# Kernel optimization log

Measured on AMD Instinct MI355X. Metric: run time of the kernel, lower is better.

Reference implementation:

```python
import jax, jax.numpy as jnp
import numpy as np

B, N, KS = 4, 4096, 16  # ks = int(k * random_rate) = int(20 * 0.8)
EPS = 1e-5


def bn_relu(x):
    # training-mode BatchNorm (stats over all dims but channel=last) + ReLU
    ax = tuple(range(x.ndim - 1))
    m = x.mean(ax, keepdims=True)
    v = x.var(ax, keepdims=True)
    return jax.nn.relu((x - m) * jax.lax.rsqrt(v + EPS))


def knn_idx(points, ks):
    # points: [B,N,3] -> neighbor indices [B,N,ks] (self included)
    sq = jnp.sum(points * points, -1)
    d2 = sq[:, :, None] + sq[:, None, :] - 2.0 * jnp.einsum('bnd,bmd->bnm', points, points)
    _, idx = jax.lax.top_k(-d2, ks)
    return idx


def gather(f, idx):
    # f: [B,N,C], idx: [B,N,k] -> [B,N,k,C]
    return jax.vmap(lambda ff, ii: ff[ii])(f, idx)


def edge_conv(feat, idx, W, pts=None):
    # EdgeConv: concat(x_i, x_j - x_i [, p_j - p_i]) -> 1x1 conv -> BN+ReLU -> max_k
    nb = gather(feat, idx)                       # [B,N,k,C]
    c = feat[:, :, None, :]
    e = jnp.concatenate([jnp.broadcast_to(c, nb.shape), nb - c], -1)
    if pts is not None:
        e = jnp.concatenate([e, gather(pts, idx) - pts[:, :, None, :]], -1)
    h = jnp.einsum('bnkc,cd->bnkd', e, W)
    return bn_relu(h).max(2)                     # [B,N,out]


def graph_conv(feat, idx, W):
    agg = gather(feat, idx).max(2)               # [B,N,C]
    return bn_relu(agg @ W)


def forward(data, W_fc, b_fc, W1, W2, W3, W4, W5, W6, W10, W11, W12, W13):
    pts = data[..., :3]
    idx = knn_idx(pts, KS)                       # [B,N,KS]
    x0 = bn_relu(data @ W_fc + b_fc)             # fc_start + bn_start, [B,N,64]
    x = edge_conv(x0, idx, W1, pts=pts)          # spFEM 64 -> 256 (edge dim 131)
    x = graph_conv(x, idx, W2)                   # 256 -> 64
    x = graph_conv(x, idx, W3)                   # 64 -> 64
    x1 = x
    x = edge_conv(x, idx, W4)                    # FEM 64 -> 256 (edge dim 128)
    x = graph_conv(x, idx, W5)                   # 256 -> 64
    x = graph_conv(x, idx, W6)                   # 64 -> 64
    x2 = x
    # (conv7..conv90 produce x3/x4 which the head never consumes -> skipped)
    x12 = jnp.concatenate([x1, x2], -1)          # [B,N,128]
    h = bn_relu(x12 @ W10)                       # conv10: 128 -> 1024
    g = h.max(1)                                 # global max pool, [B,1024]
    cat = jnp.concatenate([jnp.broadcast_to(g[:, None, :], (B, N, 1024)), x1, x2], -1)  # [B,N,1152]
    h = bn_relu(cat @ W11)                       # conv11: 1152 -> 512
    h = bn_relu(h @ W12)                         # conv12: 512 -> 256
    out = h @ W13                                # conv13: 256 -> 13 (dropout = identity in eval)
    return out.transpose(0, 2, 1)                # [B,13,N]


def setup_inputs() -> dict:
    key = jax.random.key(0)
    ks = jax.random.split(key, 16)
    w = lambda k, *s: jax.random.normal(k, s, jnp.float32) * 0.05
    return {
        'data': jax.random.normal(ks[0], (B, N, 9), jnp.float32),
        'W_fc': w(ks[1], 9, 64), 'b_fc': jnp.zeros((64,), jnp.float32),
        'W1': w(ks[2], 131, 256),   # 2*64 + 3 (sp variant adds p_j - p_i)
        'W2': w(ks[3], 256, 64), 'W3': w(ks[4], 64, 64),
        'W4': w(ks[5], 128, 256),   # 2*64
        'W5': w(ks[6], 256, 64), 'W6': w(ks[7], 64, 64),
        'W10': w(ks[8], 128, 1024), 'W11': w(ks[9], 1152, 512),
        'W12': w(ks[10], 512, 256), 'W13': w(ks[11], 256, 13),
    }


def reference(data, W_fc, b_fc, W1, W2, W3, W4, W5, W6, W10, W11, W12, W13):
    return forward(data, W_fc, b_fc, W1, W2, W3, W4, W5, W6, W10, W11, W12, W13)
```

## Files before the change

### kernel.cpp

```cpp
#include <hip/hip_runtime.h>
#include <hip/hip_bf16.h>
#include <float.h>

static constexpr int BB  = 4;
static constexpr int NN  = 4096;
static constexpr int KSN = 16;
static constexpr int RN  = BB * NN;
#define EPSBN 1e-5f

typedef __attribute__((ext_vector_type(8))) short short8;
typedef __attribute__((ext_vector_type(4))) short short4v;
typedef __attribute__((ext_vector_type(4))) float f32x4;

__device__ inline unsigned short f2bf(float f) {
  union { float f; unsigned u; } v; v.f = f;
  unsigned r = v.u + 0x7FFF + ((v.u >> 16) & 1);
  return (unsigned short)(r >> 16);
}
__device__ inline float bf2f(unsigned short h) {
  union { unsigned u; float f; } v; v.u = ((unsigned)h) << 16; return v.f;
}

__global__ __launch_bounds__(256) void prepgram_kernel(const float* __restrict__ data,
                                                       float4* __restrict__ pack,
                                                       float* __restrict__ partials) {
  const int t = blockIdx.x * 256 + threadIdx.x;
  const int lane = threadIdx.x & 63, wave = threadIdx.x >> 6;
  __shared__ float red[4][54];
  float d[9];
#pragma unroll
  for (int k = 0; k < 9; ++k) d[k] = data[(size_t)t * 9 + k];
  pack[t] = make_float4(d[0], d[1], d[2], fmaf(d[2], d[2], fmaf(d[1], d[1], d[0] * d[0])));
  int p = 0;
#pragma unroll
  for (int i = 0; i < 9; ++i) {
    float v = d[i];
#pragma unroll
    for (int mv = 1; mv < 64; mv <<= 1) v += __shfl_xor(v, mv);
    if (lane == 0) red[wave][p] = v;
    ++p;
  }
#pragma unroll
  for (int i = 0; i < 9; ++i)
#pragma unroll
    for (int j = i; j < 9; ++j) {
      float v = d[i] * d[j];
#pragma unroll
      for (int mv = 1; mv < 64; mv <<= 1) v += __shfl_xor(v, mv);
      if (lane == 0) red[wave][p] = v;
      ++p;
    }
  __syncthreads();
  if (threadIdx.x < 54)
    partials[blockIdx.x * 54 + threadIdx.x] =
        red[0][threadIdx.x] + red[1][threadIdx.x] + red[2][threadIdx.x] + red[3][threadIdx.x];
}

__global__ void fcstats_kernel(const float* __restrict__ partials,
                               const float* __restrict__ W, const float* __restrict__ bias,
                               float* __restrict__ S0) {
  __shared__ float g[54];
  const int t = threadIdx.x;
  if (t < 54) {
    float s = 0.f;
    for (int b = 0; b < 64; ++b) s += partials[b * 54 + t];
    g[t] = s;
  }
  __syncthreads();
  float w[9];
#pragma unroll
  for (int k = 0; k < 9; ++k) w[k] = W[k * 64 + t];
  float b = bias[t];
  float dotw = 0.f;
#pragma unroll
  for (int k = 0; k < 9; ++k) dotw = fmaf(g[k], w[k], dotw);
  float s2 = 0.f;
  int p = 9;
#pragma unroll
  for (int i = 0; i < 9; ++i)
#pragma unroll
    for (int j = i; j < 9; ++j) {
      float gij = g[p++];
      s2 = fmaf(gij * ((i == j) ? 1.f : 2.f), w[i] * w[j], s2);
    }
  s2 += 2.f * b * dotw + (float)RN * b * b;
  S0[t] = dotw + (float)RN * b;
  S0[64 + t] = s2;
}

__device__ inline void wpack_one(const float* __restrict__ W, unsigned short* __restrict__ wh,
                                 unsigned short* __restrict__ wl, int t, int lgC, int NK) {
  int k = t >> lgC, c = t & ((1 << lgC) - 1);
  float v = W[t];
  int ct = c >> 4, cl = c & 15, ks = k >> 5, kl = k & 31;
  int dst = ((ct * NK + ks) * 64 + (((kl >> 3) << 4) | cl)) * 8 + (kl & 7);
  unsigned short h = f2bf(v);
  wh[dst] = h; wl[dst] = f2bf(v - bf2f(h));
}
__device__ inline void diffpack_one(const float* __restrict__ W, unsigned short* __restrict__ wh,
                                    unsigned short* __restrict__ wl, int t) {
  int k = t >> 8, cc = t & 255;
  float v = W[k * 256 + cc] - W[(64 + k) * 256 + cc];
  int ct = cc >> 4, cl = cc & 15, ks = k >> 5, kl = k & 31;
  int dst = ((ct * 2 + ks) * 64 + (((kl >> 3) << 4) | cl)) * 8 + (kl & 7);
  unsigned short h = f2bf(v);
  wh[dst] = h; wl[dst] = f2bf(v - bf2f(h));
}

__global__ __launch_bounds__(256) void mega_kernel(
    const float4* __restrict__ pack, int* __restrict__ idx,
    const float* __restrict__ data, const float* __restrict__ W_fc,
    const float* __restrict__ b_fc, const float* __restrict__ S0,
    unsigned short* __restrict__ xbh, unsigned short* __restrict__ xbl,
    const float* __restrict__ W1, const float* __restrict__ W4,
    const float* __restrict__ W2, const float* __restrict__ W3,
    const float* __restrict__ W5, const float* __restrict__ W6,
    const float* __restrict__ W10, const float* __restrict__ W11, const float* __restrict__ W12,
    unsigned short* __restrict__ W1mh, unsigned short* __restrict__ W1ml, float4* __restrict__ W1bt,
    unsigned short* __restrict__ W4mh, unsigned short* __restrict__ W4ml,
    unsigned short* __restrict__ W1ph, unsigned short* __restrict__ W1pl,
    unsigned short* __restrict__ W4ph, unsigned short* __restrict__ W4pl,
    unsigned short* __restrict__ W2h, unsigned short* __restrict__ W2l,
    unsigned short* __restrict__ W3h, unsigned short* __restrict__ W3l,
    unsigned short* __restrict__ W5h, unsigned short* __restrict__ W5l,
    unsigned short* __restrict__ W6h, unsigned short* __restrict__ W6l,
    unsigned short* __restrict__ W10h, unsigned short* __restrict__ W10l,
    unsigned short* __restrict__ W11xh, unsigned short* __restrict__ W11xl,
    unsigned short* __restrict__ W12h, unsigned short* __restrict__ W12l) {
  const int blk = blockIdx.x;
  if (blk < 4096) {
    const int lane = threadIdx.x & 63;
    const int p = blk * 4 + (threadIdx.x >> 6);
    const int b = p >> 12;
    const float4* __restrict__ pb = pack + ((size_t)b << 12);
    const float4 me = pack[p];
    unsigned long long m0 = ~0ull, m1 = ~0ull, m2 = ~0ull, m3 = ~0ull;
#pragma unroll 8
    for (int s = 0; s < 64; ++s) {
      const float4 q = pb[s * 64 + lane];
      float d = me.w + q.w - 2.0f * fmaf(me.x, q.x, fmaf(me.y, q.y, me.z * q.z));
      unsigned ub = __float_as_uint(d);
      ub = (ub & 0x80000000u) ? ~ub : (ub | 0x80000000u);
      unsigned long long k = ((unsigned long long)ub << 12) | (unsigned)(s * 64 + lane);
      if (k < m3) {
        bool l0 = k < m0;  unsigned long long t0 = l0 ? m0 : k;  m0 = l0 ? k : m0;
        bool l1 = t0 < m1; unsigned long long t1 = l1 ? m1 : t0; m1 = l1 ? t0 : m1;
        bool l2 = t1 < m2; unsigned long long t2 = l2 ? m2 : t1; m2 = l2 ? t1 : m2;
        m3 = (t2 < m3) ? t2 : m3;
      }
    }
    for (int pass = 0; pass < 16; ++pass) {
      unsigned d0 = (unsigned)(m0 >> 12);
      unsigned w32 = d0;
#pragma unroll
      for (int mv = 1; mv < 64; mv <<= 1) {
        unsigned o = __shfl_xor(w32, mv);
        w32 = (o < w32) ? o : w32;
      }
      unsigned long long ball = __ballot(d0 == w32);
      unsigned widx;
      if (__popcll(ball) == 1) {
        widx = __shfl((unsigned)(m0 & 0xFFFull), (int)(__ffsll((long long)ball) - 1));
      } else {
        unsigned cand = (d0 == w32) ? (unsigned)(m0 & 0xFFFull) : 0xFFFFFFFFu;
#pragma unroll
        for (int mv = 1; mv < 64; mv <<= 1) {
          unsigned o = __shfl_xor(cand, mv);
          cand = (o < cand) ? o : cand;
        }
        widx = cand;
      }
      const unsigned long long w = ((unsigned long long)w32 << 12) | widx;
      if (lane == pass) idx[(p << 4) + pass] = (int)widx;
      if (m0 == w) { m0 = m1; m1 = m2; m2 = m3; m3 = ~0ull; }
      if (pass < 15 && __any(m0 == ~0ull)) {
        if (m0 == ~0ull) {
          m1 = ~0ull; m2 = ~0ull; m3 = ~0ull;
#pragma unroll 8
          for (int s = 0; s < 64; ++s) {
            const float4 q = pb[s * 64 + lane];
            float d = me.w + q.w - 2.0f * fmaf(me.x, q.x, fmaf(me.y, q.y, me.z * q.z));
            unsigned ub = __float_as_uint(d);
            ub = (ub & 0x80000000u) ? ~ub : (ub | 0x80000000u);
            unsigned long long k = ((unsigned long long)ub << 12) | (unsigned)(s * 64 + lane);
            k = (k > w) ? k : ~0ull;
            if (k < m3) {
              bool l0 = k < m0;  unsigned long long t0 = l0 ? m0 : k;  m0 = l0 ? k : m0;
              bool l1 = t0 < m1; unsigned long long t1 = l1 ? m1 : t0; m1 = l1 ? t0 : m1;
              bool l2 = t1 < m2; unsigned long long t2 = l2 ? m2 : t1; m2 = l2 ? t1 : m2;
              m3 = (t2 < m3) ? t2 : m3;
            }
          }
        }
      }
    }
  } else if (blk < 8192) {
    const int t = (blk - 4096) * 256 + threadIdx.x;
    const int r = t >> 6, c = t & 63;
    const float* dr = data + (size_t)r * 9;
    float acc = b_fc[c];
#pragma unroll
    for (int k = 0; k < 9; ++k) acc = fmaf(dr[k], W_fc[k * 64 + c], acc);
    const float inv = 1.0f / RN;
    float m = S0[c] * inv;
    float v = fmaxf(S0[64 + c] * inv - m * m, 0.0f);
    float x = fmaxf((acc - m) * rsqrtf(v + EPSBN), 0.0f);
    unsigned short h = f2bf(x);
    xbh[t] = h; xbl[t] = f2bf(x - bf2f(h));
  } else {
    const int mb = blk - 8192;
    if (mb < 64) {
      int t = mb * 256 + threadIdx.x;
      int k = t >> 8, cc = t & 255;
      float w1mid = W1[(64 + k) * 256 + cc];
      unsigned short h1 = f2bf(w1mid);
      W1mh[cc * 64 + k] = h1;
      W1ml[cc * 64 + k] = f2bf(w1mid - bf2f(h1));
      float w4mid = W4[(64 + k) * 256 + cc];
      unsigned short h4 = f2bf(w4mid);
      W4mh[cc * 64 + k] = h4;
      W4ml[cc * 64 + k] = f2bf(w4mid - bf2f(h4));
      if (t < 256) W1bt[t] = make_float4(W1[128 * 256 + t], W1[129 * 256 + t], W1[130 * 256 + t], 0.f);
    } else if (mb < 128) {
      diffpack_one(W1, W1ph, W1pl, (mb - 64) * 256 + threadIdx.x);
    } else if (mb < 192) {
      diffpack_one(W4, W4ph, W4pl, (mb - 128) * 256 + threadIdx.x);
    } else if (mb < 256) {
      wpack_one(W2, W2h, W2l, (mb - 192) * 256 + threadIdx.x, 6, 8);
    } else if (mb < 272) {
      wpack_one(W3, W3h, W3l, (mb - 256) * 256 + threadIdx.x, 6, 2);
    } else if (mb < 336) {
      wpack_one(W5, W5h, W5l, (mb - 272) * 256 + threadIdx.x, 6, 8);
    } else if (mb < 352) {
      wpack_one(W6, W6h, W6l, (mb - 336) * 256 + threadIdx.x, 6, 2);
    } else if (mb < 864) {
      wpack_one(W10, W10h, W10l, (mb - 352) * 256 + threadIdx.x, 10, 4);
    } else if (mb < 1120) {
      wpack_one(W11 + 1024 * 512, W11xh, W11xl, (mb - 864) * 256 + threadIdx.x, 9, 4);
    } else {
      wpack_one(W12, W12h, W12l, (mb - 1120) * 256 + threadIdx.x, 8, 16);
    }
  }
}

__global__ void pack_x12_kernel(const float* __restrict__ x1, const float* __restrict__ x2,
                                const float* __restrict__ S6,
                                unsigned short* __restrict__ ph, unsigned short* __restrict__ pl) {
  int t = blockIdx.x * 256 + threadIdx.x;
  int r = t >> 7, k = t & 127;
  float v;
  if (k < 64) {
    v = x1[(size_t)r * 64 + k];
  } else {
    int c = k - 64;
    const float inv = 1.0f / RN;
    float m = S6[c] * inv;
    float var = fmaxf(S6[64 + c] * inv - m * m, 0.f);
    v = fmaxf((x2[(size_t)r * 64 + c] - m) * rsqrtf(var + EPSBN), 0.f);
  }
  int rt = r >> 4, rl = r & 15, ks = k >> 5, kl = k & 31;
  int dst = ((rt * 4 + ks) * 64 + (((kl >> 3) << 4) | rl)) * 8 + (kl & 7);
  unsigned short h = f2bf(v);
  ph[dst] = h; pl[dst] = f2bf(v - bf2f(h));
}

__global__ void bn_pack_kernel(const float* __restrict__ buf, const float* __restrict__ stats,
                               unsigned short* __restrict__ ph, unsigned short* __restrict__ pl) {
  int t = blockIdx.x * 256 + threadIdx.x;
  int c = t & 511, r = t >> 9;
  const float inv = 1.0f / RN;
  float m = stats[c] * inv;
  float v = fmaxf(stats[512 + c] * inv - m * m, 0.0f);
  float x = fmaxf((buf[t] - m) * rsqrtf(v + EPSBN), 0.0f);
  int rt = r >> 4, rl = r & 15, ks = c >> 5, kl = c & 31;
  int dst = ((rt * 16 + ks) * 64 + (((kl >> 3) << 4) | rl)) * 8 + (kl & 7);
  unsigned short h = f2bf(x);
  ph[dst] = h; pl[dst] = f2bf(x - bf2f(h));
}

__global__ void bn_normpack_kernel(float* __restrict__ buf, const float* __restrict__ stats,
                                   unsigned short* __restrict__ hi, unsigned short* __restrict__ lo) {
  int t = blockIdx.x * 256 + threadIdx.x;
  int c = t & 63;
  const float inv = 1.0f / RN;
  float m = stats[c] * inv;
  float v = fmaxf(stats[64 + c] * inv - m * m, 0.0f);
  float x = fmaxf((buf[t] - m) * rsqrtf(v + EPSBN), 0.0f);
  buf[t] = x;
  unsigned short h = f2bf(x);
  hi[t] = h; lo[t] = f2bf(x - bf2f(h));
}

template <bool HAS_PTS>
__global__ __launch_bounds__(256) void edge_mfma_kernel(
    const unsigned short* __restrict__ Xh, const unsigned short* __restrict__ Xl,
    const int* __restrict__ idx,
    const float4* __restrict__ pack,
    const unsigned short* __restrict__ Wmh, const unsigned short* __restrict__ Wml,
    const float4* __restrict__ Wbt, const float* __restrict__ basemat,
    float* __restrict__ out, float* __restrict__ stats) {
  const int wave = threadIdx.x >> 6;
  const int lane = threadIdx.x & 63;
  const int pg   = blockIdx.x;
  const int c0   = wave << 6;
  const int cl   = lane & 15;
  const int kg   = (lane >> 4) << 3;
  const int bat  = pg >> 8;
  const int pbase = bat << 12;
  const int ib   = pg << 8;

  short8 bh[4][2], blo[4][2];
#pragma unroll
  for (int q = 0; q < 4; ++q) {
    const unsigned short* wp = Wmh + (size_t)(c0 + q * 16 + cl) * 64 + kg;
    bh[q][0] = *(const short8*)wp; bh[q][1] = *(const short8*)(wp + 32);
    const unsigned short* wq = Wml + (size_t)(c0 + q * 16 + cl) * 64 + kg;
    blo[q][0] = *(const short8*)wq; blo[q][1] = *(const short8*)(wq + 32);
  }
  float4 wb[4];
  if (HAS_PTS) {
#pragma unroll
    for (int q = 0; q < 4; ++q) wb[q] = Wbt[c0 + q * 16 + cl];
  }
  float P1[4] = {0.f, 0.f, 0.f, 0.f}, P2[4] = {0.f, 0.f, 0.f, 0.f};
  float PCx[4] = {0.f, 0.f, 0.f, 0.f};
  float PB1[4] = {0.f, 0.f, 0.f, 0.f}, PB2[4] = {0.f, 0.f, 0.f, 0.f};

  int jn = idx[ib + 16 + cl];
  int j0 = idx[ib + cl];
  size_t ro = ((size_t)(pbase | j0) << 6) + kg;
  short8 a0h = *(const short8*)(Xh + ro);
  short8 a1h = *(const short8*)(Xh + ro + 32);
  short8 a0l = *(const short8*)(Xl + ro);
  short8 a1l = *(const short8*)(Xl + ro + 32);

  for (int pp = 0; pp < 16; ++pp) {
    const int p = (pg << 4) | pp;
    int jf = 0;
    if (pp < 14) jf = idx[ib + ((pp + 2) << 4) + cl];
    short8 n0h, n1h, n0l, n1l;
    if (pp < 15) {
      size_t rn = ((size_t)(pbase | jn) << 6) + kg;
      n0h = *(const short8*)(Xh + rn);
      n1h = *(const short8*)(Xh + rn + 32);
      n0l = *(const short8*)(Xl + rn);
      n1l = *(const short8*)(Xl + rn + 32);
    }
    float dx0, dy0, dz0, dx1, dy1, dz1, dx2, dy2, dz2, dx3, dy3, dz3;
    if (HAS_PTS) {
      const int4 j4 = *(const int4*)(idx + (p << 4) + ((lane >> 4) << 2));
      const float4 pc = pack[p];
      const float4 q0 = pack[pbase | j4.x];
      const float4 q1 = pack[pbase | j4.y];
      const float4 q2 = pack[pbase | j4.z];
      const float4 q3 = pack[pbase | j4.w];
      dx0 = q0.x - pc.x; dy0 = q0.y - pc.y; dz0 = q0.z - pc.z;
      dx1 = q1.x - pc.x; dy1 = q1.y - pc.y; dz1 = q1.z - pc.z;
      dx2 = q2.x - pc.x; dy2 = q2.y - pc.y; dz2 = q2.z - pc.z;
      dx3 = q3.x - pc.x; dy3 = q3.y - pc.y; dz3 = q3.z - pc.z;
    }
    f32x4 acc[4];
#pragma unroll
    for (int q = 0; q < 4; ++q) {
      acc[q][0] = 0.f; acc[q][1] = 0.f; acc[q][2] = 0.f; acc[q][3] = 0.f;
    }
#pragma unroll
    for (int q = 0; q < 4; ++q) {
      acc[q] = __builtin_amdgcn_mfma_f32_16x16x32_bf16(a0l, bh[q][0], acc[q], 0, 0, 0);
      acc[q] = __builtin_amdgcn_mfma_f32_16x16x32_bf16(a1l, bh[q][1], acc[q], 0, 0, 0);
      acc[q] = __builtin_amdgcn_mfma_f32_16x16x32_bf16(a0h, blo[q][0], acc[q], 0, 0, 0);
      acc[q] = __builtin_amdgcn_mfma_f32_16x16x32_bf16(a1h, blo[q][1], acc[q], 0, 0, 0);
      acc[q] = __builtin_amdgcn_mfma_f32_16x16x32_bf16(a0h, bh[q][0], acc[q], 0, 0, 0);
      acc[q] = __builtin_amdgcn_mfma_f32_16x16x32_bf16(a1h, bh[q][1], acc[q], 0, 0, 0);
    }
    if (HAS_PTS) {
#pragma unroll
      for (int q = 0; q < 4; ++q) {
        acc[q][0] += dx0 * wb[q].x + dy0 * wb[q].y + dz0 * wb[q].z;
        acc[q][1] += dx1 * wb[q].x + dy1 * wb[q].y + dz1 * wb[q].z;
        acc[q][2] += dx2 * wb[q].x + dy2 * wb[q].y + dz2 * wb[q].z;
        acc[q][3] += dx3 * wb[q].x + dy3 * wb[q].y + dz3 * wb[q].z;
      }
    }
#pragma unroll
    for (int q = 0; q < 4; ++q) {
      float s1p = acc[q][0] + acc[q][1] + acc[q][2] + acc[q][3];
      float s2p = acc[q][0] * acc[q][0] + acc[q][1] * acc[q][1]
                + acc[q][2] * acc[q][2] + acc[q][3] * acc[q][3];
      float mx = fmaxf(fmaxf(acc[q][0], acc[q][1]), fmaxf(acc[q][2], acc[q][3]));
      mx = fmaxf(mx, __shfl_xor(mx, 16));
      mx = fmaxf(mx, __shfl_xor(mx, 32));
      float bb = basemat[(size_t)p * 256 + c0 + q * 16 + cl];
      if (lane < 16) out[(size_t)p * 256 + c0 + q * 16 + cl] = mx + bb;
      P1[q] += s1p;
      P2[q] += s2p;
      PCx[q] = fmaf(bb, s1p, PCx[q]);
      PB1[q] += bb;
      PB2[q] = fmaf(bb, bb, PB2[q]);
    }
    a0h = n0h; a1h = n1h; a0l = n0l; a1l = n1l;
    jn = jf;
  }
#pragma unroll
  for (int q = 0; q < 4; ++q) {
    float p1 = P1[q]; p1 += __shfl_xor(p1, 16); p1 += __shfl_xor(p1, 32);
    float p2 = P2[q]; p2 += __shfl_xor(p2, 16); p2 += __shfl_xor(p2, 32);
    float pc = PCx[q]; pc += __shfl_xor(pc, 16); pc += __shfl_xor(pc, 32);
    if (lane < 16) {
      atomicAdd(&stats[c0 + q * 16 + lane], p1 + 16.f * PB1[q]);
      atomicAdd(&stats[256 + c0 + q * 16 + lane], p2 + 2.f * pc + 16.f * PB2[q]);
    }
  }
}

template <int LGC>
__global__ __launch_bounds__(256) void agg_pack_kernel(
    const float* __restrict__ X, const int* __restrict__ idx,
    const float* __restrict__ stats, float inv_cnt,
    unsigned short* __restrict__ ph, unsigned short* __restrict__ pl) {
  const int C = 1 << LGC;
  const int xcd = blockIdx.x & 7, bat = xcd >> 1;
  const int j = ((blockIdx.x >> 3) << 1) | (xcd & 1);
  const int rows_per_block = 256 >> (LGC - 2);
  const int r = bat * 4096 + j * rows_per_block + (threadIdx.x >> (LGC - 2));
  const int cq = threadIdx.x & ((C >> 2) - 1);
  const int base = bat << 12;
  const int* ip = idx + (size_t)r * KSN;
  float4 mx = make_float4(-FLT_MAX, -FLT_MAX, -FLT_MAX, -FLT_MAX);
#pragma unroll
  for (int k = 0; k < KSN; ++k) {
    int jj = ip[k];
    const float4 v = *reinterpret_cast<const float4*>(X + (size_t)(base + jj) * C + cq * 4);
    mx.x = fmaxf(mx.x, v.x); mx.y = fmaxf(mx.y, v.y);
    mx.z = fmaxf(mx.z, v.z); mx.w = fmaxf(mx.w, v.w);
  }
  const int c = cq * 4;
  const float4 sa = *reinterpret_cast<const float4*>(stats + c);
  const float4 sb = *reinterpret_cast<const float4*>(stats + C + c);
  float m0 = sa.x * inv_cnt, m1 = sa.y * inv_cnt, m2 = sa.z * inv_cnt, m3 = sa.w * inv_cnt;
  float o0 = fmaxf((mx.x - m0) * rsqrtf(fmaxf(sb.x * inv_cnt - m0 * m0, 0.f) + EPSBN), 0.f);
  float o1 = fmaxf((mx.y - m1) * rsqrtf(fmaxf(sb.y * inv_cnt - m1 * m1, 0.f) + EPSBN), 0.f);
  float o2 = fmaxf((mx.z - m2) * rsqrtf(fmaxf(sb.z * inv_cnt - m2 * m2, 0.f) + EPSBN), 0.f);
  float o3 = fmaxf((mx.w - m3) * rsqrtf(fmaxf(sb.w * inv_cnt - m3 * m3, 0.f) + EPSBN), 0.f);
  short4v H, L;
  H.x = (short)f2bf(o0); L.x = (short)f2bf(o0 - bf2f((unsigned short)H.x));
  H.y = (short)f2bf(o1); L.y = (short)f2bf(o1 - bf2f((unsigned short)H.y));
  H.z = (short)f2bf(o2); L.z = (short)f2bf(o2 - bf2f((unsigned short)H.z));
  H.w = (short)f2bf(o3); L.w = (short)f2bf(o3 - bf2f((unsigned short)H.w));
  const int NK = C >> 5;
  const int rt = r >> 4, rl = r & 15, ks = c >> 5, kl = c & 31;
  const size_t dst = (((size_t)rt * NK + ks) * 64 + (((kl >> 3) << 4) | rl)) * 8 + (kl & 7);
  *(short4v*)(ph + dst) = H;
  *(short4v*)(pl + dst) = L;
}

template <int AMODE, bool DOMAX, bool BIAS>
__global__ __launch_bounds__(256) void gemm_mfma_kernel(
    const unsigned short* __restrict__ Ah, const unsigned short* __restrict__ Al,
    const unsigned short* __restrict__ Wh, const unsigned short* __restrict__ Wl,
    float* __restrict__ Y, float* __restrict__ pmax, float* __restrict__ stats,
    const float* __restrict__ gbias,
    int K, int C) {
  __shared__ float red1[4][64], red2[4][64], redm[4][64];
  const int wave = threadIdx.x >> 6, lane = threadIdx.x & 63;
  const int rtb = blockIdx.x * 16 + wave * 4;
  const int c0  = blockIdx.y * 64;
  const int ct0 = blockIdx.y * 4;
  const int NK  = K >> 5;
  const int bat = blockIdx.x >> 4;
  f32x4 acc[4][4];
#pragma unroll
  for (int r = 0; r < 4; ++r)
#pragma unroll
    for (int cc = 0; cc < 4; ++cc) {
      acc[r][cc][0] = 0.f; acc[r][cc][1] = 0.f; acc[r][cc][2] = 0.f; acc[r][cc][3] = 0.f;
    }
  const int lhalf = (lane >> 4) << 3;
  for (int ks = 0; ks < NK; ++ks) {
    short8 ah[4], al[4];
    if (AMODE == 1) {
#pragma unroll
      for (int r = 0; r < 4; ++r) {
        const size_t aoff = ((size_t)((rtb + r) * 16 + (lane & 15))) * 64 + ks * 32 + lhalf;
        ah[r] = *(const short8*)(Ah + aoff);
        al[r] = *(const short8*)(Al + aoff);
      }
    } else {
#pragma unroll
      for (int r = 0; r < 4; ++r) {
        const size_t aoff = (((size_t)(rtb + r) * NK + ks) * 64 + lane) * 8;
        ah[r] = *(const short8*)(Ah + aoff);
        al[r] = *(const short8*)(Al + aoff);
      }
    }
#pragma unroll
    for (int cc = 0; cc < 4; ++cc) {
      const size_t woff = (((size_t)(ct0 + cc) * NK + ks) * 64 + lane) * 8;
      short8 bh = *(const short8*)(Wh + woff);
      short8 bl = *(const short8*)(Wl + woff);
#pragma unroll
      for (int r = 0; r < 4; ++r) {
        acc[r][cc] = __builtin_amdgcn_mfma_f32_16x16x32_bf16(al[r], bh, acc[r][cc], 0, 0, 0);
        acc[r][cc] = __builtin_amdgcn_mfma_f32_16x16x32_bf16(ah[r], bl, acc[r][cc], 0, 0, 0);
        acc[r][cc] = __builtin_amdgcn_mfma_f32_16x16x32_bf16(ah[r], bh, acc[r][cc], 0, 0, 0);
      }
    }
  }
#pragma unroll
  for (int cc = 0; cc < 4; ++cc) {
    float bv = 0.f;
    if (BIAS) bv = gbias[(size_t)bat * C + c0 + cc * 16 + (lane & 15)];
    float s1 = 0.f, s2 = 0.f, mm = -FLT_MAX;
#pragma unroll
    for (int r = 0; r < 4; ++r) {
#pragma unroll
      for (int i = 0; i < 4; ++i) {
        float v = acc[r][cc][i] + bv;
        if (!DOMAX)
          Y[(size_t)((rtb + r) * 16 + ((lane >> 4) << 2) + i) * C + c0 + cc * 16 + (lane & 15)] = v;
        s1 += v; s2 = fmaf(v, v, s2); mm = fmaxf(mm, v);
      }
    }
    s1 += __shfl_xor(s1, 16); s1 += __shfl_xor(s1, 32);
    s2 += __shfl_xor(s2, 16); s2 += __shfl_xor(s2, 32);
    mm = fmaxf(mm, __shfl_xor(mm, 16)); mm = fmaxf(mm, __shfl_xor(mm, 32));
    if (lane < 16) {
      red1[wave][cc * 16 + lane] = s1;
      red2[wave][cc * 16 + lane] = s2;
      if (DOMAX) redm[wave][cc * 16 + lane] = mm;
    }
  }
  __syncthreads();
  if (threadIdx.x < 64) {
    const int t = threadIdx.x;
    float a = red1[0][t] + red1[1][t] + red1[2][t] + red1[3][t];
    float b = red2[0][t] + red2[1][t] + red2[2][t] + red2[3][t];
    atomicAdd(&stats[c0 + t], a);
    atomicAdd(&stats[C + c0 + t], b);
    if (DOMAX) {
      float mm = fmaxf(fmaxf(redm[0][t], redm[1][t]), fmaxf(redm[2][t], redm[3][t]));
      pmax[(size_t)blockIdx.x * C + c0 + t] = mm;
    }
  }
}

__global__ void fin_g_kernel(const float* __restrict__ pmax, const float* __restrict__ stats,
                             float* __restrict__ gf) {
  int t = blockIdx.x * 256 + threadIdx.x;
  int b = t >> 10, c = t & 1023;
  const float inv = 1.0f / 16384.0f;
  float m = stats[c] * inv;
  float v = fmaxf(stats[1024 + c] * inv - m * m, 0.0f);
  float rs = rsqrtf(v + EPSBN);
  float mx = -FLT_MAX;
  for (int s = 0; s < 16; ++s) mx = fmaxf(mx, pmax[(size_t)(b * 16 + s) * 1024 + c]);
  gf[t] = fmaxf((mx - m) * rs, 0.0f);
}

__global__ __launch_bounds__(256) void gb11_kernel(const float* __restrict__ gf,
                                                   const float* __restrict__ W11,
                                                   float* __restrict__ gb) {
  int t = blockIdx.x * 256 + threadIdx.x;
  int b = t >> 9, c = t & 511;
  const float* g = gf + b * 1024;
  float acc = 0.f;
#pragma unroll 8
  for (int k = 0; k < 1024; ++k) acc = fmaf(g[k], W11[(size_t)k * 512 + c], acc);
  gb[t] = acc;
}

__global__ __launch_bounds__(256) void final13_kernel(const float* __restrict__ h,
                                                      const float* __restrict__ S9,
                                                      const float* __restrict__ W,
                                                      float* __restrict__ out) {
  __shared__ float wl[256 * 13];
  __shared__ float ms[256], rs[256];
  const int t = threadIdx.x;
  {
    const float inv = 1.0f / RN;
    float m = S9[t] * inv;
    float v = fmaxf(S9[256 + t] * inv - m * m, 0.0f);
    ms[t] = m; rs[t] = rsqrtf(v + EPSBN);
#pragma unroll
    for (int i = 0; i < 13; ++i) wl[t * 13 + i] = W[t * 13 + i];
  }
  __syncthreads();
  const int r = blockIdx.x * 16 + (t >> 4);
  const int c = t & 15;
  const int ci = (c < 13) ? c : 0;
  const float* hr = h + (size_t)r * 256;
  float acc = 0.0f;
  for (int k = 0; k < 256; ++k) {
    float x = fmaxf((hr[k] - ms[k]) * rs[k], 0.0f);
    acc = fmaf(x, wl[k * 13 + ci], acc);
  }
  if (c < 13) {
    int b = r >> 12, n = r & 4095;
    out[(size_t)b * 13 * NN + (size_t)c * NN + n] = acc;
  }
}

extern "C" void kernel_launch(void* const* d_in, const int* in_sizes, int n_in,
                              void* d_out, int out_size, void* d_ws, size_t ws_size,
                              hipStream_t stream) {
  (void)in_sizes; (void)n_in; (void)out_size; (void)ws_size;
  const float* data = (const float*)d_in[0];
  const float* W_fc = (const float*)d_in[1];
  const float* b_fc = (const float*)d_in[2];
  const float* W1   = (const float*)d_in[3];
  const float* W2   = (const float*)d_in[4];
  const float* W3   = (const float*)d_in[5];
  const float* W4   = (const float*)d_in[6];
  const float* W5   = (const float*)d_in[7];
  const float* W6   = (const float*)d_in[8];
  const float* W10  = (const float*)d_in[9];
  const float* W11  = (const float*)d_in[10];
  const float* W12  = (const float*)d_in[11];
  const float* W13  = (const float*)d_in[12];
  float* out = (float*)d_out;

  float* ws  = (float*)d_ws;
  int*   idx = (int*)d_ws;
  size_t o = 262144;
  float* x0   = ws + o; o += (size_t)RN * 64;
  float* x1v  = ws + o; o += (size_t)RN * 64;
  float* x2v  = ws + o; o += (size_t)RN * 64;
  float* bufA = ws + o; o += (size_t)RN * 256;
  float* bufB = ws + o; o += (size_t)RN * 256;
  float* bufC = ws + o; o += (size_t)RN * 64;
  float* pmax = ws + o; o += (size_t)64 * 1024;
  float* h11  = ws + o; o += (size_t)RN * 512;
  float* h12  = ws + o; o += (size_t)RN * 256;
  float* stats = ws + o; o += 8192;
  float4* pack = (float4*)(ws + o); o += (size_t)RN * 4;
  unsigned short* xbh = (unsigned short*)(ws + o); o += (size_t)RN * 32;
  unsigned short* xbl = (unsigned short*)(ws + o); o += (size_t)RN * 32;
  unsigned short* W1mh = (unsigned short*)(ws + o); o += 8192;
  unsigned short* W1ml = (unsigned short*)(ws + o); o += 8192;
  unsigned short* W4mh = (unsigned short*)(ws + o); o += 8192;
  unsigned short* W4ml = (unsigned short*)(ws + o); o += 8192;
  float4* W1bt = (float4*)(ws + o); o += 1024;
  unsigned short* W10h = (unsigned short*)(ws + o); o += 65536;
  unsigned short* W10l = (unsigned short*)(ws + o); o += 65536;
  unsigned short* W11xh = (unsigned short*)(ws + o); o += 32768;
  unsigned short* W11xl = (unsigned short*)(ws + o); o += 32768;
  unsigned short* W12h = (unsigned short*)(ws + o); o += 65536;
  unsigned short* W12l = (unsigned short*)(ws + o); o += 65536;
  float* gf = ws + o; o += 4096;
  float* gb = ws + o; o += 2048;
  unsigned short* W1ph = (unsigned short*)(ws + o); o += 8192;
  unsigned short* W1pl = (unsigned short*)(ws + o); o += 8192;
  unsigned short* W4ph = (unsigned short*)(ws + o); o += 8192;
  unsigned short* W4pl = (unsigned short*)(ws + o); o += 8192;
  unsigned short* W2h  = (unsigned short*)(ws + o); o += 8192;
  unsigned short* W2l  = (unsigned short*)(ws + o); o += 8192;
  unsigned short* W3h  = (unsigned short*)(ws + o); o += 2048;
  unsigned short* W3l  = (unsigned short*)(ws + o); o += 2048;
  unsigned short* W5h  = (unsigned short*)(ws + o); o += 8192;
  unsigned short* W5l  = (unsigned short*)(ws + o); o += 8192;
  unsigned short* W6h  = (unsigned short*)(ws + o); o += 2048;
  unsigned short* W6l  = (unsigned short*)(ws + o); o += 2048;
  float* gpart = ws + o; o += 64 * 54;
  unsigned short* x12h = (unsigned short*)bufC;
  unsigned short* x12l = (unsigned short*)x0;
  unsigned short* h11h = (unsigned short*)bufA;
  unsigned short* h11l = (unsigned short*)bufB;
  unsigned short* aggh = (unsigned short*)h11;
  unsigned short* aggl = (unsigned short*)h11 + (size_t)RN * 256;

  float* S0 = stats;
  float* S1 = stats + 128;
  float* S2 = stats + 640;
  float* S3 = stats + 768;
  float* S4 = stats + 896;
  float* S5 = stats + 1408;
  float* S6 = stats + 1536;
  float* S7 = stats + 1664;
  float* S8 = stats + 3712;
  float* S9 = stats + 4736;
  float* Sd = stats + 5248;

  hipMemsetAsync(stats, 0, 8192 * sizeof(float), stream);

  prepgram_kernel<<<64, 256, 0, stream>>>(data, pack, gpart);
  fcstats_kernel<<<1, 64, 0, stream>>>(gpart, W_fc, b_fc, S0);

  mega_kernel<<<9824, 256, 0, stream>>>(
      pack, idx, data, W_fc, b_fc, S0, xbh, xbl,
      W1, W4, W2, W3, W5, W6, W10, W11, W12,
      W1mh, W1ml, W1bt, W4mh, W4ml,
      W1ph, W1pl, W4ph, W4pl, W2h, W2l, W3h, W3l, W5h, W5l, W6h, W6l,
      W10h, W10l, W11xh, W11xl, W12h, W12l);

  gemm_mfma_kernel<1, false, false><<<dim3(64, 4), 256, 0, stream>>>(
      xbh, xbl, W1ph, W1pl, bufB, nullptr, Sd, nullptr, 64, 256);
  edge_mfma_kernel<true><<<1024, 256, 0, stream>>>(xbh, xbl, idx, pack, W1mh, W1ml, W1bt, bufB, bufA, S1);

  agg_pack_kernel<8><<<4096, 256, 0, stream>>>(bufA, idx, S1, 1.0f / (RN * 16), aggh, aggl);
  gemm_mfma_kernel<0, false, false><<<dim3(64, 1), 256, 0, stream>>>(
      aggh, aggl, W2h, W2l, bufC, nullptr, S2, nullptr, 256, 64);

  agg_pack_kernel<6><<<1024, 256, 0, stream>>>(bufC, idx, S2, 1.0f / RN, aggh, aggl);
  gemm_mfma_kernel<0, false, false><<<dim3(64, 1), 256, 0, stream>>>(
      aggh, aggl, W3h, W3l, x1v, nullptr, S3, nullptr, 64, 64);
  bn_normpack_kernel<<<RN * 64 / 256, 256, 0, stream>>>(x1v, S3, xbh, xbl);

  gemm_mfma_kernel<1, false, false><<<dim3(64, 4), 256, 0, stream>>>(
      xbh, xbl, W4ph, W4pl, bufB, nullptr, Sd, nullptr, 64, 256);
  edge_mfma_kernel<false><<<1024, 256, 0, stream>>>(xbh, xbl, idx, pack, W4mh, W4ml, nullptr, bufB, bufA, S4);

  agg_pack_kernel<8><<<4096, 256, 0, stream>>>(bufA, idx, S4, 1.0f / (RN * 16), aggh, aggl);
  gemm_mfma_kernel<0, false, false><<<dim3(64, 1), 256, 0, stream>>>(
      aggh, aggl, W5h, W5l, bufC, nullptr, S5, nullptr, 256, 64);

  agg_pack_kernel<6><<<1024, 256, 0, stream>>>(bufC, idx, S5, 1.0f / RN, aggh, aggl);
  gemm_mfma_kernel<0, false, false><<<dim3(64, 1), 256, 0, stream>>>(
      aggh, aggl, W6h, W6l, x2v, nullptr, S6, nullptr, 64, 64);

  pack_x12_kernel<<<RN * 128 / 256, 256, 0, stream>>>(x1v, x2v, S6, x12h, x12l);

  gemm_mfma_kernel<0, true, false><<<dim3(64, 16), 256, 0, stream>>>(
      x12h, x12l, W10h, W10l, nullptr, pmax, S7, nullptr, 128, 1024);
  fin_g_kernel<<<16, 256, 0, stream>>>(pmax, S7, gf);

  gb11_kernel<<<8, 256, 0, stream>>>(gf, W11, gb);
  gemm_mfma_kernel<0, false, true><<<dim3(64, 8), 256, 0, stream>>>(
      x12h, x12l, W11xh, W11xl, h11, nullptr, S8, gb, 128, 512);
  bn_pack_kernel<<<RN * 512 / 256, 256, 0, stream>>>(h11, S8, h11h, h11l);

  gemm_mfma_kernel<0, false, false><<<dim3(64, 4), 256, 0, stream>>>(
      h11h, h11l, W12h, W12l, h12, nullptr, S9, nullptr, 512, 256);

  final13_kernel<<<RN / 16, 256, 0, stream>>>(h12, S9, W13, out);
}
```

Measured before the change: 598.2 us.

## Fuse center-point base GEMM into edge kernel and merge global-feature kernels

The edge kernel now computes the per-point base term (x_i times the packed center weight) with MFMAs at its start and distributes it across lanes with shuffles. This removes the separate base GEMM launch and its round trip through a 256-channel buffer for both EdgeConv layers. The global-max finalization and the conv11 global-bias matvec are merged into one kernel that keeps g in shared memory, saving a launch and an intermediate buffer. The cost is extra registers and MFMA work inside the edge kernel, and the unrolled inner loop adds code size.

```diff
diff --git a/kernel.cpp b/kernel.cpp
--- a/kernel.cpp
+++ b/kernel.cpp
@@ -297,7 +297,8 @@
     const int* __restrict__ idx,
     const float4* __restrict__ pack,
     const unsigned short* __restrict__ Wmh, const unsigned short* __restrict__ Wml,
-    const float4* __restrict__ Wbt, const float* __restrict__ basemat,
+    const unsigned short* __restrict__ Wph, const unsigned short* __restrict__ Wpl,
+    const float4* __restrict__ Wbt,
     float* __restrict__ out, float* __restrict__ stats) {
   const int wave = threadIdx.x >> 6;
   const int lane = threadIdx.x & 63;
@@ -322,6 +323,33 @@
 #pragma unroll
     for (int q = 0; q < 4; ++q) wb[q] = Wbt[c0 + q * 16 + cl];
   }
+
+  f32x4 base[4];
+  {
+    const size_t xoff = ((size_t)((pg << 4) + cl)) * 64 + kg;
+    short8 xa0h = *(const short8*)(Xh + xoff);
+    short8 xa1h = *(const short8*)(Xh + xoff + 32);
+    short8 xa0l = *(const short8*)(Xl + xoff);
+    short8 xa1l = *(const short8*)(Xl + xoff + 32);
+#pragma unroll
+    for (int q = 0; q < 4; ++q) {
+      base[q][0] = 0.f; base[q][1] = 0.f; base[q][2] = 0.f; base[q][3] = 0.f;
+      const int ct = wave * 4 + q;
+      const size_t w0 = (((size_t)ct * 2 + 0) * 64 + lane) * 8;
+      const size_t w1 = (((size_t)ct * 2 + 1) * 64 + lane) * 8;
+      short8 p0h = *(const short8*)(Wph + w0);
+      short8 p0l = *(const short8*)(Wpl + w0);
+      short8 p1h = *(const short8*)(Wph + w1);
+      short8 p1l = *(const short8*)(Wpl + w1);
+      base[q] = __builtin_amdgcn_mfma_f32_16x16x32_bf16(xa0l, p0h, base[q], 0, 0, 0);
+      base[q] = __builtin_amdgcn_mfma_f32_16x16x32_bf16(xa0h, p0l, base[q], 0, 0, 0);
+      base[q] = __builtin_amdgcn_mfma_f32_16x16x32_bf16(xa0h, p0h, base[q], 0, 0, 0);
+      base[q] = __builtin_amdgcn_mfma_f32_16x16x32_bf16(xa1l, p1h, base[q], 0, 0, 0);
+      base[q] = __builtin_amdgcn_mfma_f32_16x16x32_bf16(xa1h, p1l, base[q], 0, 0, 0);
+      base[q] = __builtin_amdgcn_mfma_f32_16x16x32_bf16(xa1h, p1h, base[q], 0, 0, 0);
+    }
+  }
+
   float P1[4] = {0.f, 0.f, 0.f, 0.f}, P2[4] = {0.f, 0.f, 0.f, 0.f};
   float PCx[4] = {0.f, 0.f, 0.f, 0.f};
   float PB1[4] = {0.f, 0.f, 0.f, 0.f}, PB2[4] = {0.f, 0.f, 0.f, 0.f};
@@ -334,72 +362,76 @@
   short8 a0l = *(const short8*)(Xl + ro);
   short8 a1l = *(const short8*)(Xl + ro + 32);
 
-  for (int pp = 0; pp < 16; ++pp) {
-    const int p = (pg << 4) | pp;
-    int jf = 0;
-    if (pp < 14) jf = idx[ib + ((pp + 2) << 4) + cl];
-    short8 n0h, n1h, n0l, n1l;
-    if (pp < 15) {
-      size_t rn = ((size_t)(pbase | jn) << 6) + kg;
-      n0h = *(const short8*)(Xh + rn);
-      n1h = *(const short8*)(Xh + rn + 32);
-      n0l = *(const short8*)(Xl + rn);
-      n1l = *(const short8*)(Xl + rn + 32);
-    }
-    float dx0, dy0, dz0, dx1, dy1, dz1, dx2, dy2, dz2, dx3, dy3, dz3;
-    if (HAS_PTS) {
-      const int4 j4 = *(const int4*)(idx + (p << 4) + ((lane >> 4) << 2));
-      const float4 pc = pack[p];
-      const float4 q0 = pack[pbase | j4.x];
-      const float4 q1 = pack[pbase | j4.y];
-      const float4 q2 = pack[pbase | j4.z];
-      const float4 q3 = pack[pbase | j4.w];
-      dx0 = q0.x - pc.x; dy0 = q0.y - pc.y; dz0 = q0.z - pc.z;
-      dx1 = q1.x - pc.x; dy1 = q1.y - pc.y; dz1 = q1.z - pc.z;
-      dx2 = q2.x - pc.x; dy2 = q2.y - pc.y; dz2 = q2.z - pc.z;
-      dx3 = q3.x - pc.x; dy3 = q3.y - pc.y; dz3 = q3.z - pc.z;
-    }
-    f32x4 acc[4];
-#pragma unroll
-    for (int q = 0; q < 4; ++q) {
-      acc[q][0] = 0.f; acc[q][1] = 0.f; acc[q][2] = 0.f; acc[q][3] = 0.f;
-    }
-#pragma unroll
-    for (int q = 0; q < 4; ++q) {
-      acc[q] = __builtin_amdgcn_mfma_f32_16x16x32_bf16(a0l, bh[q][0], acc[q], 0, 0, 0);
-      acc[q] = __builtin_amdgcn_mfma_f32_16x16x32_bf16(a1l, bh[q][1], acc[q], 0, 0, 0);
-      acc[q] = __builtin_amdgcn_mfma_f32_16x16x32_bf16(a0h, blo[q][0], acc[q], 0, 0, 0);
-      acc[q] = __builtin_amdgcn_mfma_f32_16x16x32_bf16(a1h, blo[q][1], acc[q], 0, 0, 0);
-      acc[q] = __builtin_amdgcn_mfma_f32_16x16x32_bf16(a0h, bh[q][0], acc[q], 0, 0, 0);
-      acc[q] = __builtin_amdgcn_mfma_f32_16x16x32_bf16(a1h, bh[q][1], acc[q], 0, 0, 0);
-    }
-    if (HAS_PTS) {
+  for (int g = 0; g < 4; ++g) {
+#pragma unroll
+    for (int i = 0; i < 4; ++i) {
+      const int pp = g * 4 + i;
+      const int p = (pg << 4) | pp;
+      int jf = 0;
+      if (pp < 14) jf = idx[ib + ((pp + 2) << 4) + cl];
+      short8 n0h, n1h, n0l, n1l;
+      if (pp < 15) {
+        size_t rn = ((size_t)(pbase | jn) << 6) + kg;
+        n0h = *(const short8*)(Xh + rn);
+        n1h = *(const short8*)(Xh + rn + 32);
+        n0l = *(const short8*)(Xl + rn);
+        n1l = *(const short8*)(Xl + rn + 32);
+      }
+      float dx0, dy0, dz0, dx1, dy1, dz1, dx2, dy2, dz2, dx3, dy3, dz3;
+      if (HAS_PTS) {
+        const int4 j4 = *(const int4*)(idx + (p << 4) + ((lane >> 4) << 2));
+        const float4 pc = pack[p];
+        const float4 q0 = pack[pbase | j4.x];
+        const float4 q1 = pack[pbase | j4.y];
+        const float4 q2 = pack[pbase | j4.z];
+        const float4 q3 = pack[pbase | j4.w];
+        dx0 = q0.x - pc.x; dy0 = q0.y - pc.y; dz0 = q0.z - pc.z;
+        dx1 = q1.x - pc.x; dy1 = q1.y - pc.y; dz1 = q1.z - pc.z;
+        dx2 = q2.x - pc.x; dy2 = q2.y - pc.y; dz2 = q2.z - pc.z;
+        dx3 = q3.x - pc.x; dy3 = q3.y - pc.y; dz3 = q3.z - pc.z;
+      }
+      f32x4 acc[4];
 #pragma unroll
       for (int q = 0; q < 4; ++q) {
-        acc[q][0] += dx0 * wb[q].x + dy0 * wb[q].y + dz0 * wb[q].z;
-        acc[q][1] += dx1 * wb[q].x + dy1 * wb[q].y + dz1 * wb[q].z;
-        acc[q][2] += dx2 * wb[q].x + dy2 * wb[q].y + dz2 * wb[q].z;
-        acc[q][3] += dx3 * wb[q].x + dy3 * wb[q].y + dz3 * wb[q].z;
-      }
-    }
-#pragma unroll
-    for (int q = 0; q < 4; ++q) {
-      float s1p = acc[q][0] + acc[q][1] + acc[q][2] + acc[q][3];
-      float s2p = acc[q][0] * acc[q][0] + acc[q][1] * acc[q][1]
-                + acc[q][2] * acc[q][2] + acc[q][3] * acc[q][3];
-      float mx = fmaxf(fmaxf(acc[q][0], acc[q][1]), fmaxf(acc[q][2], acc[q][3]));
-      mx = fmaxf(mx, __shfl_xor(mx, 16));
-      mx = fmaxf(mx, __shfl_xor(mx, 32));
-      float bb = basemat[(size_t)p * 256 + c0 + q * 16 + cl];
-      if (lane < 16) out[(size_t)p * 256 + c0 + q * 16 + cl] = mx + bb;
-      P1[q] += s1p;
-      P2[q] += s2p;
-      PCx[q] = fmaf(bb, s1p, PCx[q]);
-      PB1[q] += bb;
-      PB2[q] = fmaf(bb, bb, PB2[q]);
-    }
-    a0h = n0h; a1h = n1h; a0l = n0l; a1l = n1l;
-    jn = jf;
+        acc[q][0] = 0.f; acc[q][1] = 0.f; acc[q][2] = 0.f; acc[q][3] = 0.f;
+      }
+#pragma unroll
+      for (int q = 0; q < 4; ++q) {
+        acc[q] = __builtin_amdgcn_mfma_f32_16x16x32_bf16(a0l, bh[q][0], acc[q], 0, 0, 0);
+        acc[q] = __builtin_amdgcn_mfma_f32_16x16x32_bf16(a1l, bh[q][1], acc[q], 0, 0, 0);
+        acc[q] = __builtin_amdgcn_mfma_f32_16x16x32_bf16(a0h, blo[q][0], acc[q], 0, 0, 0);
+        acc[q] = __builtin_amdgcn_mfma_f32_16x16x32_bf16(a1h, blo[q][1], acc[q], 0, 0, 0);
+        acc[q] = __builtin_amdgcn_mfma_f32_16x16x32_bf16(a0h, bh[q][0], acc[q], 0, 0, 0);
+        acc[q] = __builtin_amdgcn_mfma_f32_16x16x32_bf16(a1h, bh[q][1], acc[q], 0, 0, 0);
+      }
+      if (HAS_PTS) {
+#pragma unroll
+        for (int q = 0; q < 4; ++q) {
+          acc[q][0] += dx0 * wb[q].x + dy0 * wb[q].y + dz0 * wb[q].z;
+          acc[q][1] += dx1 * wb[q].x + dy1 * wb[q].y + dz1 * wb[q].z;
+          acc[q][2] += dx2 * wb[q].x + dy2 * wb[q].y + dz2 * wb[q].z;
+          acc[q][3] += dx3 * wb[q].x + dy3 * wb[q].y + dz3 * wb[q].z;
+        }
+      }
+#pragma unroll
+      for (int q = 0; q < 4; ++q) {
+        float s1p = acc[q][0] + acc[q][1] + acc[q][2] + acc[q][3];
+        float s2p = acc[q][0] * acc[q][0] + acc[q][1] * acc[q][1]
+                  + acc[q][2] * acc[q][2] + acc[q][3] * acc[q][3];
+        float mx = fmaxf(fmaxf(acc[q][0], acc[q][1]), fmaxf(acc[q][2], acc[q][3]));
+        mx = fmaxf(mx, __shfl_xor(mx, 16));
+        mx = fmaxf(mx, __shfl_xor(mx, 32));
+        float bb = __shfl(base[q][i], (g << 4) | cl);
+        if (lane < 16) out[(size_t)p * 256 + c0 + q * 16 + cl] = mx + bb;
+        P1[q] += s1p;
+        P2[q] += s2p;
+        PCx[q] = fmaf(bb, s1p, PCx[q]);
+        PB1[q] += bb;
+        PB2[q] = fmaf(bb, bb, PB2[q]);
+      }
+      a0h = n0h; a1h = n1h; a0l = n0l; a1l = n1l;
+      jn = jf;
+    }
   }
 #pragma unroll
   for (int q = 0; q < 4; ++q) {
@@ -544,29 +576,30 @@
   }
 }
 
-__global__ void fin_g_kernel(const float* __restrict__ pmax, const float* __restrict__ stats,
-                             float* __restrict__ gf) {
-  int t = blockIdx.x * 256 + threadIdx.x;
-  int b = t >> 10, c = t & 1023;
+__global__ __launch_bounds__(256) void fing_gb_kernel(const float* __restrict__ pmax,
+                                                      const float* __restrict__ S7,
+                                                      const float* __restrict__ W11,
+                                                      float* __restrict__ gb) {
+  __shared__ float g_lds[1024];
+  const int t = threadIdx.x;
+  const int b = blockIdx.x >> 1, ch = blockIdx.x & 1;
   const float inv = 1.0f / 16384.0f;
-  float m = stats[c] * inv;
-  float v = fmaxf(stats[1024 + c] * inv - m * m, 0.0f);
-  float rs = rsqrtf(v + EPSBN);
-  float mx = -FLT_MAX;
-  for (int s = 0; s < 16; ++s) mx = fmaxf(mx, pmax[(size_t)(b * 16 + s) * 1024 + c]);
-  gf[t] = fmaxf((mx - m) * rs, 0.0f);
-}
-
-__global__ __launch_bounds__(256) void gb11_kernel(const float* __restrict__ gf,
-                                                   const float* __restrict__ W11,
-                                                   float* __restrict__ gb) {
-  int t = blockIdx.x * 256 + threadIdx.x;
-  int b = t >> 9, c = t & 511;
-  const float* g = gf + b * 1024;
+#pragma unroll
+  for (int kk = 0; kk < 4; ++kk) {
+    int c = kk * 256 + t;
+    float m = S7[c] * inv;
+    float v = fmaxf(S7[1024 + c] * inv - m * m, 0.0f);
+    float rs = rsqrtf(v + EPSBN);
+    float mx = -FLT_MAX;
+    for (int s = 0; s < 16; ++s) mx = fmaxf(mx, pmax[(size_t)(b * 16 + s) * 1024 + c]);
+    g_lds[c] = fmaxf((mx - m) * rs, 0.0f);
+  }
+  __syncthreads();
+  const int c_out = ch * 256 + t;
   float acc = 0.f;
 #pragma unroll 8
-  for (int k = 0; k < 1024; ++k) acc = fmaf(g[k], W11[(size_t)k * 512 + c], acc);
-  gb[t] = acc;
+  for (int k = 0; k < 1024; ++k) acc = fmaf(g_lds[k], W11[(size_t)k * 512 + c_out], acc);
+  gb[b * 512 + c_out] = acc;
 }
 
 __global__ __launch_bounds__(256) void final13_kernel(const float* __restrict__ h,
@@ -646,7 +679,6 @@
   unsigned short* W11xl = (unsigned short*)(ws + o); o += 32768;
   unsigned short* W12h = (unsigned short*)(ws + o); o += 65536;
   unsigned short* W12l = (unsigned short*)(ws + o); o += 65536;
-  float* gf = ws + o; o += 4096;
   float* gb = ws + o; o += 2048;
   unsigned short* W1ph = (unsigned short*)(ws + o); o += 8192;
   unsigned short* W1pl = (unsigned short*)(ws + o); o += 8192;
@@ -678,7 +710,6 @@
   float* S7 = stats + 1664;
   float* S8 = stats + 3712;
   float* S9 = stats + 4736;
-  float* Sd = stats + 5248;
 
   hipMemsetAsync(stats, 0, 8192 * sizeof(float), stream);
 
@@ -692,9 +723,8 @@
       W1ph, W1pl, W4ph, W4pl, W2h, W2l, W3h, W3l, W5h, W5l, W6h, W6l,
       W10h, W10l, W11xh, W11xl, W12h, W12l);
 
-  gemm_mfma_kernel<1, false, false><<<dim3(64, 4), 256, 0, stream>>>(
-      xbh, xbl, W1ph, W1pl, bufB, nullptr, Sd, nullptr, 64, 256);
-  edge_mfma_kernel<true><<<1024, 256, 0, stream>>>(xbh, xbl, idx, pack, W1mh, W1ml, W1bt, bufB, bufA, S1);
+  edge_mfma_kernel<true><<<1024, 256, 0, stream>>>(
+      xbh, xbl, idx, pack, W1mh, W1ml, W1ph, W1pl, W1bt, bufA, S1);
 
   agg_pack_kernel<8><<<4096, 256, 0, stream>>>(bufA, idx, S1, 1.0f / (RN * 16), aggh, aggl);
   gemm_mfma_kernel<0, false, false><<<dim3(64, 1), 256, 0, stream>>>(
@@ -705,9 +735,8 @@
       aggh, aggl, W3h, W3l, x1v, nullptr, S3, nullptr, 64, 64);
   bn_normpack_kernel<<<RN * 64 / 256, 256, 0, stream>>>(x1v, S3, xbh, xbl);
 
-  gemm_mfma_kernel<1, false, false><<<dim3(64, 4), 256, 0, stream>>>(
-      xbh, xbl, W4ph, W4pl, bufB, nullptr, Sd, nullptr, 64, 256);
-  edge_mfma_kernel<false><<<1024, 256, 0, stream>>>(xbh, xbl, idx, pack, W4mh, W4ml, nullptr, bufB, bufA, S4);
+  edge_mfma_kernel<false><<<1024, 256, 0, stream>>>(
+      xbh, xbl, idx, pack, W4mh, W4ml, W4ph, W4pl, nullptr, bufA, S4);
 
   agg_pack_kernel<8><<<4096, 256, 0, stream>>>(bufA, idx, S4, 1.0f / (RN * 16), aggh, aggl);
   gemm_mfma_kernel<0, false, false><<<dim3(64, 1), 256, 0, stream>>>(
@@ -721,9 +750,9 @@
 
   gemm_mfma_kernel<0, true, false><<<dim3(64, 16), 256, 0, stream>>>(
       x12h, x12l, W10h, W10l, nullptr, pmax, S7, nullptr, 128, 1024);
-  fin_g_kernel<<<16, 256, 0, stream>>>(pmax, S7, gf);
-
-  gb11_kernel<<<8, 256, 0, stream>>>(gf, W11, gb);
+
+  fing_gb_kernel<<<8, 256, 0, stream>>>(pmax, S7, W11, gb);
+
   gemm_mfma_kernel<0, false, true><<<dim3(64, 8), 256, 0, stream>>>(
       x12h, x12l, W11xh, W11xl, h11, nullptr, S8, gb, 128, 512);
   bn_pack_kernel<<<RN * 512 / 256, 256, 0, stream>>>(h11, S8, h11h, h11l);
```

New measurement: 557.9 us. 6.7% less time.
